# Performance work log

Measured on AMD Instinct MI355X. Metric: run time of the kernel, lower is better.

## Reference

```python
import jax, jax.numpy as jnp
import numpy as np

B, D, H = 524288, 256, 4
DH = D // H
LN_EPS = 1e-5


def setup_inputs() -> dict:
    key = jax.random.key(0)
    ks = jax.random.split(key, 3)
    s = 0.02  # typical init scale
    return {
        "x": jax.random.normal(ks[0], (B, 2, D), dtype=jnp.float32),
        "in_proj_w": jax.random.normal(ks[1], (3 * D, D), dtype=jnp.float32) * s,
        "in_proj_b": jnp.zeros((3 * D,), dtype=jnp.float32),
        "out_proj_w": jax.random.normal(ks[2], (D, D), dtype=jnp.float32) * s,
        "out_proj_b": jnp.zeros((D,), dtype=jnp.float32),
        "ln_gamma": jnp.ones((D,), dtype=jnp.float32),
        "ln_beta": jnp.zeros((D,), dtype=jnp.float32),
    }


def _mha_1to1(q, k, v, Wq, bq, Wk, bk, Wv, bv, Wo, bo):
    # q, k, v: [B, D]  (seq_len == 1 collapsed). Faithful MHA math.
    Q = (q @ Wq.T + bq).reshape(-1, H, DH)  # [B,H,DH]
    K = (k @ Wk.T + bk).reshape(-1, H, DH)
    V = (v @ Wv.T + bv).reshape(-1, H, DH)
    scores = jnp.sum(Q * K, axis=-1, keepdims=True) / np.sqrt(DH)  # [B,H,1]
    w = jax.nn.softmax(scores, axis=-1)  # softmax over a single key -> 1
    out = (w * V).reshape(-1, D)  # [B,D]
    return out @ Wo.T + bo


def reference(x, in_proj_w, in_proj_b, out_proj_w, out_proj_b, ln_gamma, ln_beta):
    Wq, Wk, Wv = jnp.split(in_proj_w, 3, axis=0)
    bq, bk, bv = jnp.split(in_proj_b, 3, axis=0)
    x0, x1 = x[:, 0, :], x[:, 1, :]
    out12 = _mha_1to1(x0, x1, x1, Wq, bq, Wk, bk, Wv, bv, out_proj_w, out_proj_b)
    out21 = _mha_1to1(x1, x0, x0, Wq, bq, Wk, bk, Wv, bv, out_proj_w, out_proj_b)
    fused = jnp.stack([out12, out21], axis=1)  # [B,2,D]
    y = x + fused  # dropout = identity in eval
    mu = jnp.mean(y, axis=-1, keepdims=True)
    var = jnp.var(y, axis=-1, keepdims=True)
    return (y - mu) * jax.lax.rsqrt(var + LN_EPS) * ln_gamma + ln_beta
```

## Files before the change

kernel.cpp:

```cpp
#include <hip/hip_runtime.h>

#define DD 256
#define TOTROWS (524288 * 2)
#define NBLOCKS 256
#define RPI 32
#define ITERS (TOTROWS / (NBLOCKS * RPI))
#define XROW 528
#define XBUF(i) ((i) * (RPI * XROW))
#define YBUF(i) (4 * RPI * XROW + (i) * (RPI * XROW))
#define LDS_TOTAL (6 * RPI * XROW)

typedef __attribute__((ext_vector_type(8))) short short8;
typedef __attribute__((ext_vector_type(4))) float f32x4;
typedef __attribute__((ext_vector_type(4))) unsigned short u16x4;

__device__ inline unsigned short f2bf(float x) {
    unsigned u = __builtin_bit_cast(unsigned, x);
    u += 0x7fffu + ((u >> 16) & 1u);
    return (unsigned short)(u >> 16);
}
__device__ inline float bf2f(unsigned short h) {
    unsigned u = ((unsigned)h) << 16;
    return __builtin_bit_cast(float, u);
}

__device__ inline void block_sync_lds() {
    __builtin_amdgcn_sched_barrier(0);
    asm volatile("s_waitcnt lgkmcnt(0)" ::: "memory");
    __builtin_amdgcn_s_barrier();
    __builtin_amdgcn_sched_barrier(0);
}

__global__ void wprep_kernel(const float* __restrict__ in_w,
                             const float* __restrict__ in_b,
                             const float* __restrict__ out_w,
                             const float* __restrict__ out_b,
                             unsigned short* __restrict__ Wbf,
                             float* __restrict__ cvec) {
    __shared__ float worow[DD];
    __shared__ float part[DD];
    const int i = blockIdx.x;
    const int j = threadIdx.x;
    worow[j] = out_w[i * DD + j];
    __syncthreads();
    const float* wv = in_w + 512 * DD;
    float s = 0.f;
    for (int k = 0; k < DD; ++k) s = fmaf(worow[k], wv[k * DD + j], s);
    Wbf[i * DD + j] = f2bf(s);
    part[j] = worow[j] * in_b[512 + j];
    __syncthreads();
    if (j == 0) {
        float c = out_b[i];
        for (int k = 0; k < DD; ++k) c += part[k];
        cvec[i] = c;
    }
}

__global__ __launch_bounds__(512, 2) void fused_kernel(
    const float* __restrict__ x, const unsigned short* __restrict__ Wbf,
    const float* __restrict__ cvec, const float* __restrict__ gamma,
    const float* __restrict__ beta, float* __restrict__ out) {
    extern __shared__ __align__(16) char lds[];
    const int tid = threadIdx.x;
    const int w = tid >> 6, lane = tid & 63;
    const int m = lane & 15, g = lane >> 4;
    const int lc = lane & 15, lr = tid >> 4;

    short8 af[2][8];
#pragma unroll
    for (int n2 = 0; n2 < 2; ++n2)
#pragma unroll
        for (int s = 0; s < 8; ++s)
            af[n2][s] = *(const short8*)(Wbf + (w * 32 + n2 * 16 + m) * 256 + s * 32 + g * 8);

    f32x4 creg[2];
#pragma unroll
    for (int n2 = 0; n2 < 2; ++n2)
        creg[n2] = *(const f32x4*)(cvec + w * 32 + n2 * 16 + g * 4);
    f32x4 gg[4], bb[4];
#pragma unroll
    for (int k = 0; k < 4; ++k) {
        gg[k] = *(const f32x4*)(gamma + lc * 4 + k * 64);
        bb[k] = *(const f32x4*)(beta + lc * 4 + k * 64);
    }

    const size_t rowbase = (size_t)blockIdx.x * (ITERS * RPI);

    f32x4 svA[4], svB[4];
#pragma unroll
    for (int j = 0; j < 4; ++j)
        svA[j] = *(const f32x4*)(x + rowbase * DD + j * 2048 + tid * 4);
#pragma unroll
    for (int j = 0; j < 4; ++j) {
        const int row = j * 8 + w;
        u16x4 h = {f2bf(svA[j][0]), f2bf(svA[j][1]), f2bf(svA[j][2]), f2bf(svA[j][3])};
        *(u16x4*)(lds + XBUF(0) + row * XROW + lane * 8) = h;
    }
#pragma unroll
    for (int j = 0; j < 4; ++j)
        svA[j] = *(const f32x4*)(x + (rowbase + RPI) * DD + j * 2048 + tid * 4);
#pragma unroll
    for (int j = 0; j < 4; ++j) {
        const int row = j * 8 + w;
        u16x4 h = {f2bf(svA[j][0]), f2bf(svA[j][1]), f2bf(svA[j][2]), f2bf(svA[j][3])};
        *(u16x4*)(lds + XBUF(1) + row * XROW + lane * 8) = h;
    }
#pragma unroll
    for (int j = 0; j < 4; ++j)
        svA[j] = *(const f32x4*)(x + (rowbase + 2 * RPI) * DD + j * 2048 + tid * 4);
    block_sync_lds();

#define REGION(IT, SVC, SVN)                                                     \
    {                                                                            \
        const int it = (IT);                                                     \
        const int xbc = XBUF(it & 3);                                            \
        const int xbs = XBUF((it + 2) & 3);                                      \
        const int ybA = YBUF(it & 1);                                            \
        const int ybB = YBUF((it + 1) & 1);                                      \
        const size_t r0 = rowbase + (size_t)it * RPI;                            \
                                           \
        if (it > 0) {                                                            \
            const size_t rp = r0 - RPI + lr;                                     \
            u16x4 yh[4];                                                         \
            _Pragma("unroll")                                                    \
            for (int k = 0; k < 4; ++k)                                          \
                yh[k] = *(const u16x4*)(lds + ybB + lr * XROW + lc * 8 + k * 128);\
            float s1 = 0.f, s2 = 0.f;                                            \
            float f[4][4];                                                       \
            _Pragma("unroll")                                                    \
            for (int k = 0; k < 4; ++k)                                          \
                _Pragma("unroll")                                                \
                for (int e = 0; e < 4; ++e) {                                    \
                    float v = bf2f(yh[k][e]);                                    \
                    f[k][e] = v;                                                 \
                    s1 += v;                                                     \
                    s2 = fmaf(v, v, s2);                                         \
                }                                                                \
            s1 += __shfl_xor(s1, 1); s2 += __shfl_xor(s2, 1);                    \
            s1 += __shfl_xor(s1, 2); s2 += __shfl_xor(s2, 2);                    \
            s1 += __shfl_xor(s1, 4); s2 += __shfl_xor(s2, 4);                    \
            s1 += __shfl_xor(s1, 8); s2 += __shfl_xor(s2, 8);                    \
            const float mu = s1 * (1.f / 256.f);                                 \
            const float var = s2 * (1.f / 256.f) - mu * mu;                      \
            const float rs = rsqrtf(var + 1e-5f);                                \
            _Pragma("unroll")                                                    \
            for (int k = 0; k < 4; ++k) {                                        \
                f32x4 o;                                                         \
                _Pragma("unroll")                                                \
                for (int e = 0; e < 4; ++e)                                      \
                    o[e] = fmaf((f[k][e] - mu) * rs, gg[k][e], bb[k][e]);        \
                __builtin_nontemporal_store(o, (f32x4*)(out + rp * DD + lc * 4 + k * 64)); \
            }                                                                    \
        }                                                                        \
                        \
        f32x4 acc[2][2];                                                         \
        acc[0][0] = f32x4{0.f, 0.f, 0.f, 0.f};                                   \
        acc[0][1] = f32x4{0.f, 0.f, 0.f, 0.f};                                   \
        acc[1][0] = f32x4{0.f, 0.f, 0.f, 0.f};                                   \
        acc[1][1] = f32x4{0.f, 0.f, 0.f, 0.f};                                   \
        _Pragma("unroll")                                                        \
        for (int t = 0; t < 2; ++t) {                                            \
            const int rowp = t * 16 + (m ^ 1);                                   \
            const char* bbase = lds + xbc + rowp * XROW + g * 16;                \
            _Pragma("unroll")                                                    \
            for (int s = 0; s < 8; ++s) {                                        \
                short8 bf_ = *(const short8*)(bbase + s * 64);                   \
                acc[t][0] = __builtin_amdgcn_mfma_f32_16x16x32_bf16(af[0][s], bf_, acc[t][0], 0, 0, 0); \
                acc[t][1] = __builtin_amdgcn_mfma_f32_16x16x32_bf16(af[1][s], bf_, acc[t][1], 0, 0, 0); \
            }                                                                    \
        }                                                                        \
        _Pragma("unroll")                                                        \
        for (int t = 0; t < 2; ++t) {                                            \
            const int rowm = t * 16 + m;                                         \
            _Pragma("unroll")                                                    \
            for (int n2 = 0; n2 < 2; ++n2) {                                     \
                u16x4 rh = *(const u16x4*)(lds + xbc + rowm * XROW + w * 64 + n2 * 32 + g * 8); \
                f32x4 y = acc[t][n2];                                            \
                _Pragma("unroll")                                                \
                for (int i = 0; i < 4; ++i) y[i] += bf2f(rh[i]) + creg[n2][i];   \
                u16x4 hy = {f2bf(y[0]), f2bf(y[1]), f2bf(y[2]), f2bf(y[3])};     \
                *(u16x4*)(lds + ybA + rowm * XROW + w * 64 + n2 * 32 + g * 8) = hy; \
            }                                                                    \
        }                                                                        \
                                           \
        if (it + 2 < ITERS) {                                                    \
            _Pragma("unroll")                                                    \
            for (int j = 0; j < 4; ++j) {                                        \
                const int row = j * 8 + w;                                       \
                u16x4 h = {f2bf(SVC[j][0]), f2bf(SVC[j][1]), f2bf(SVC[j][2]), f2bf(SVC[j][3])}; \
                *(u16x4*)(lds + xbs + row * XROW + lane * 8) = h;                \
            }                                                                    \
        }                                                                        \
                   \
        if (it + 3 < ITERS) {                                                    \
            _Pragma("unroll")                                                    \
            for (int j = 0; j < 4; ++j)                                          \
                SVN[j] = *(const f32x4*)(x + (r0 + 3 * RPI) * DD + j * 2048 + tid * 4); \
        }                                                                        \
        block_sync_lds();                                                        \
    }

    for (int itb = 0; itb < ITERS; itb += 2) {
        REGION(itb, svA, svB);
        REGION(itb + 1, svB, svA);
    }
#undef REGION

    {
        const int ybB = YBUF((ITERS - 1) & 1);
        const size_t rp = rowbase + (size_t)(ITERS - 1) * RPI + lr;
        u16x4 yh[4];
#pragma unroll
        for (int k = 0; k < 4; ++k)
            yh[k] = *(const u16x4*)(lds + ybB + lr * XROW + lc * 8 + k * 128);
        float s1 = 0.f, s2 = 0.f;
        float f[4][4];
#pragma unroll
        for (int k = 0; k < 4; ++k)
#pragma unroll
            for (int e = 0; e < 4; ++e) {
                float v = bf2f(yh[k][e]);
                f[k][e] = v;
                s1 += v;
                s2 = fmaf(v, v, s2);
            }
        s1 += __shfl_xor(s1, 1); s2 += __shfl_xor(s2, 1);
        s1 += __shfl_xor(s1, 2); s2 += __shfl_xor(s2, 2);
        s1 += __shfl_xor(s1, 4); s2 += __shfl_xor(s2, 4);
        s1 += __shfl_xor(s1, 8); s2 += __shfl_xor(s2, 8);
        const float mu = s1 * (1.f / 256.f);
        const float var = s2 * (1.f / 256.f) - mu * mu;
        const float rs = rsqrtf(var + 1e-5f);
#pragma unroll
        for (int k = 0; k < 4; ++k) {
            f32x4 o;
#pragma unroll
            for (int e = 0; e < 4; ++e)
                o[e] = fmaf((f[k][e] - mu) * rs, gg[k][e], bb[k][e]);
            __builtin_nontemporal_store(o, (f32x4*)(out + rp * DD + lc * 4 + k * 64));
        }
    }
}

extern "C" void kernel_launch(void* const* d_in, const int* in_sizes, int n_in,
                              void* d_out, int out_size, void* d_ws, size_t ws_size,
                              hipStream_t stream) {
    const float* x     = (const float*)d_in[0];
    const float* in_w  = (const float*)d_in[1];
    const float* in_b  = (const float*)d_in[2];
    const float* out_w = (const float*)d_in[3];
    const float* out_b = (const float*)d_in[4];
    const float* gamma = (const float*)d_in[5];
    const float* beta  = (const float*)d_in[6];
    float* out = (float*)d_out;

    unsigned short* Wbf = (unsigned short*)d_ws;
    float* cvec = (float*)((char*)d_ws + 131072);

    hipLaunchKernelGGL(wprep_kernel, dim3(256), dim3(256), 0, stream,
                       in_w, in_b, out_w, out_b, Wbf, cvec);

    hipFuncSetAttribute(reinterpret_cast<const void*>(fused_kernel),
                        hipFuncAttributeMaxDynamicSharedMemorySize, LDS_TOTAL);
    hipLaunchKernelGGL(fused_kernel, dim3(NBLOCKS), dim3(512), LDS_TOTAL, stream,
                       x, Wbf, cvec, gamma, beta, out);
}
```

Baseline: 419.2 us.

## Stagger per-wave-pair phase order to overlap LN, MFMA, staging and loads

Each iteration's four phases (LayerNorm output, MFMA projection, bf16 staging into LDS, global prefetch) are split into macros. Each pair of waves (grp = tid>>7) runs them in a different rotated order, so at any moment different waves hit different units (VMEM, MFMA, LDS, VALU). The aim is to avoid every wave contending for the same resource at once between barriers. The switch makes the code larger and can raise register pressure, and the loop only stays correct because all four orders remain inside the same barrier region.

```diff
diff --git a/kernel.cpp b/kernel.cpp
--- a/kernel.cpp
+++ b/kernel.cpp
@@ -63,6 +63,7 @@
     extern __shared__ __align__(16) char lds[];
     const int tid = threadIdx.x;
     const int w = tid >> 6, lane = tid & 63;
+    const int grp = tid >> 7;
     const int m = lane & 15, g = lane >> 4;
     const int lc = lane & 15, lr = tid >> 4;
 
@@ -109,6 +110,91 @@
     for (int j = 0; j < 4; ++j)
         svA[j] = *(const f32x4*)(x + (rowbase + 2 * RPI) * DD + j * 2048 + tid * 4);
     block_sync_lds();
+
+#define P_LN                                                                     \
+    if (it > 0) {                                                                \
+        const size_t rp = r0 - RPI + lr;                                         \
+        u16x4 yh[4];                                                             \
+        _Pragma("unroll")                                                        \
+        for (int k = 0; k < 4; ++k)                                              \
+            yh[k] = *(const u16x4*)(lds + ybB + lr * XROW + lc * 8 + k * 128);   \
+        float s1 = 0.f, s2 = 0.f;                                                \
+        float fv[4][4];                                                          \
+        _Pragma("unroll")                                                        \
+        for (int k = 0; k < 4; ++k)                                              \
+            _Pragma("unroll")                                                    \
+            for (int e = 0; e < 4; ++e) {                                        \
+                float v = bf2f(yh[k][e]);                                        \
+                fv[k][e] = v;                                                    \
+                s1 += v;                                                         \
+                s2 = fmaf(v, v, s2);                                             \
+            }                                                                    \
+        s1 += __shfl_xor(s1, 1); s2 += __shfl_xor(s2, 1);                        \
+        s1 += __shfl_xor(s1, 2); s2 += __shfl_xor(s2, 2);                        \
+        s1 += __shfl_xor(s1, 4); s2 += __shfl_xor(s2, 4);                        \
+        s1 += __shfl_xor(s1, 8); s2 += __shfl_xor(s2, 8);                        \
+        const float mu = s1 * (1.f / 256.f);                                     \
+        const float var = s2 * (1.f / 256.f) - mu * mu;                          \
+        const float rs = rsqrtf(var + 1e-5f);                                    \
+        _Pragma("unroll")                                                        \
+        for (int k = 0; k < 4; ++k) {                                            \
+            f32x4 o;                                                             \
+            _Pragma("unroll")                                                    \
+            for (int e = 0; e < 4; ++e)                                          \
+                o[e] = fmaf((fv[k][e] - mu) * rs, gg[k][e], bb[k][e]);           \
+            __builtin_nontemporal_store(o, (f32x4*)(out + rp * DD + lc * 4 + k * 64)); \
+        }                                                                        \
+    }
+
+#define P_MFMA                                                                   \
+    {                                                                            \
+        f32x4 acc[2][2];                                                         \
+        acc[0][0] = f32x4{0.f, 0.f, 0.f, 0.f};                                   \
+        acc[0][1] = f32x4{0.f, 0.f, 0.f, 0.f};                                   \
+        acc[1][0] = f32x4{0.f, 0.f, 0.f, 0.f};                                   \
+        acc[1][1] = f32x4{0.f, 0.f, 0.f, 0.f};                                   \
+        _Pragma("unroll")                                                        \
+        for (int t = 0; t < 2; ++t) {                                            \
+            const int rowp = t * 16 + (m ^ 1);                                   \
+            const char* bbase = lds + xbc + rowp * XROW + g * 16;                \
+            _Pragma("unroll")                                                    \
+            for (int s = 0; s < 8; ++s) {                                        \
+                short8 bf_ = *(const short8*)(bbase + s * 64);                   \
+                acc[t][0] = __builtin_amdgcn_mfma_f32_16x16x32_bf16(af[0][s], bf_, acc[t][0], 0, 0, 0); \
+                acc[t][1] = __builtin_amdgcn_mfma_f32_16x16x32_bf16(af[1][s], bf_, acc[t][1], 0, 0, 0); \
+            }                                                                    \
+        }                                                                        \
+        _Pragma("unroll")                                                        \
+        for (int t = 0; t < 2; ++t) {                                            \
+            const int rowm = t * 16 + m;                                         \
+            _Pragma("unroll")                                                    \
+            for (int n2 = 0; n2 < 2; ++n2) {                                     \
+                u16x4 rh = *(const u16x4*)(lds + xbc + rowm * XROW + w * 64 + n2 * 32 + g * 8); \
+                f32x4 y = acc[t][n2];                                            \
+                _Pragma("unroll")                                                \
+                for (int i = 0; i < 4; ++i) y[i] += bf2f(rh[i]) + creg[n2][i];   \
+                u16x4 hy = {f2bf(y[0]), f2bf(y[1]), f2bf(y[2]), f2bf(y[3])};     \
+                *(u16x4*)(lds + ybA + rowm * XROW + w * 64 + n2 * 32 + g * 8) = hy; \
+            }                                                                    \
+        }                                                                        \
+    }
+
+#define P_STAGE(SVC)                                                             \
+    if (it + 2 < ITERS) {                                                        \
+        _Pragma("unroll")                                                        \
+        for (int j = 0; j < 4; ++j) {                                            \
+            const int row = j * 8 + w;                                           \
+            u16x4 h = {f2bf(SVC[j][0]), f2bf(SVC[j][1]), f2bf(SVC[j][2]), f2bf(SVC[j][3])}; \
+            *(u16x4*)(lds + xbs + row * XROW + lane * 8) = h;                    \
+        }                                                                        \
+    }
+
+#define P_LOAD(SVN)                                                              \
+    if (it + 3 < ITERS) {                                                        \
+        _Pragma("unroll")                                                        \
+        for (int j = 0; j < 4; ++j)                                              \
+            SVN[j] = *(const f32x4*)(x + (r0 + 3 * RPI) * DD + j * 2048 + tid * 4); \
+    }
 
 #define REGION(IT, SVC, SVN)                                                     \
     {                                                                            \
@@ -118,84 +204,11 @@
         const int ybA = YBUF(it & 1);                                            \
         const int ybB = YBUF((it + 1) & 1);                                      \
         const size_t r0 = rowbase + (size_t)it * RPI;                            \
-                                           \
-        if (it > 0) {                                                            \
-            const size_t rp = r0 - RPI + lr;                                     \
-            u16x4 yh[4];                                                         \
-            _Pragma("unroll")                                                    \
-            for (int k = 0; k < 4; ++k)                                          \
-                yh[k] = *(const u16x4*)(lds + ybB + lr * XROW + lc * 8 + k * 128);\
-            float s1 = 0.f, s2 = 0.f;                                            \
-            float f[4][4];                                                       \
-            _Pragma("unroll")                                                    \
-            for (int k = 0; k < 4; ++k)                                          \
-                _Pragma("unroll")                                                \
-                for (int e = 0; e < 4; ++e) {                                    \
-                    float v = bf2f(yh[k][e]);                                    \
-                    f[k][e] = v;                                                 \
-                    s1 += v;                                                     \
-                    s2 = fmaf(v, v, s2);                                         \
-                }                                                                \
-            s1 += __shfl_xor(s1, 1); s2 += __shfl_xor(s2, 1);                    \
-            s1 += __shfl_xor(s1, 2); s2 += __shfl_xor(s2, 2);                    \
-            s1 += __shfl_xor(s1, 4); s2 += __shfl_xor(s2, 4);                    \
-            s1 += __shfl_xor(s1, 8); s2 += __shfl_xor(s2, 8);                    \
-            const float mu = s1 * (1.f / 256.f);                                 \
-            const float var = s2 * (1.f / 256.f) - mu * mu;                      \
-            const float rs = rsqrtf(var + 1e-5f);                                \
-            _Pragma("unroll")                                                    \
-            for (int k = 0; k < 4; ++k) {                                        \
-                f32x4 o;                                                         \
-                _Pragma("unroll")                                                \
-                for (int e = 0; e < 4; ++e)                                      \
-                    o[e] = fmaf((f[k][e] - mu) * rs, gg[k][e], bb[k][e]);        \
-                __builtin_nontemporal_store(o, (f32x4*)(out + rp * DD + lc * 4 + k * 64)); \
-            }                                                                    \
-        }                                                                        \
-                        \
-        f32x4 acc[2][2];                                                         \
-        acc[0][0] = f32x4{0.f, 0.f, 0.f, 0.f};                                   \
-        acc[0][1] = f32x4{0.f, 0.f, 0.f, 0.f};                                   \
-        acc[1][0] = f32x4{0.f, 0.f, 0.f, 0.f};                                   \
-        acc[1][1] = f32x4{0.f, 0.f, 0.f, 0.f};                                   \
-        _Pragma("unroll")                                                        \
-        for (int t = 0; t < 2; ++t) {                                            \
-            const int rowp = t * 16 + (m ^ 1);                                   \
-            const char* bbase = lds + xbc + rowp * XROW + g * 16;                \
-            _Pragma("unroll")                                                    \
-            for (int s = 0; s < 8; ++s) {                                        \
-                short8 bf_ = *(const short8*)(bbase + s * 64);                   \
-                acc[t][0] = __builtin_amdgcn_mfma_f32_16x16x32_bf16(af[0][s], bf_, acc[t][0], 0, 0, 0); \
-                acc[t][1] = __builtin_amdgcn_mfma_f32_16x16x32_bf16(af[1][s], bf_, acc[t][1], 0, 0, 0); \
-            }                                                                    \
-        }                                                                        \
-        _Pragma("unroll")                                                        \
-        for (int t = 0; t < 2; ++t) {                                            \
-            const int rowm = t * 16 + m;                                         \
-            _Pragma("unroll")                                                    \
-            for (int n2 = 0; n2 < 2; ++n2) {                                     \
-                u16x4 rh = *(const u16x4*)(lds + xbc + rowm * XROW + w * 64 + n2 * 32 + g * 8); \
-                f32x4 y = acc[t][n2];                                            \
-                _Pragma("unroll")                                                \
-                for (int i = 0; i < 4; ++i) y[i] += bf2f(rh[i]) + creg[n2][i];   \
-                u16x4 hy = {f2bf(y[0]), f2bf(y[1]), f2bf(y[2]), f2bf(y[3])};     \
-                *(u16x4*)(lds + ybA + rowm * XROW + w * 64 + n2 * 32 + g * 8) = hy; \
-            }                                                                    \
-        }                                                                        \
-                                           \
-        if (it + 2 < ITERS) {                                                    \
-            _Pragma("unroll")                                                    \
-            for (int j = 0; j < 4; ++j) {                                        \
-                const int row = j * 8 + w;                                       \
-                u16x4 h = {f2bf(SVC[j][0]), f2bf(SVC[j][1]), f2bf(SVC[j][2]), f2bf(SVC[j][3])}; \
-                *(u16x4*)(lds + xbs + row * XROW + lane * 8) = h;                \
-            }                                                                    \
-        }                                                                        \
-                   \
-        if (it + 3 < ITERS) {                                                    \
-            _Pragma("unroll")                                                    \
-            for (int j = 0; j < 4; ++j)                                          \
-                SVN[j] = *(const f32x4*)(x + (r0 + 3 * RPI) * DD + j * 2048 + tid * 4); \
+        switch (grp) {                                                           \
+            case 0: { P_LN } P_MFMA P_STAGE(SVC) P_LOAD(SVN) break;              \
+            case 1: P_MFMA P_STAGE(SVC) P_LOAD(SVN) { P_LN } break;              \
+            case 2: P_STAGE(SVC) P_LOAD(SVN) { P_LN } P_MFMA break;              \
+            default: P_LOAD(SVN) { P_LN } P_MFMA P_STAGE(SVC) break;             \
         }                                                                        \
         block_sync_lds();                                                        \
     }
@@ -205,6 +218,10 @@
         REGION(itb + 1, svB, svA);
     }
 #undef REGION
+#undef P_LN
+#undef P_MFMA
+#undef P_STAGE
+#undef P_LOAD
 
     {
         const int ybB = YBUF((ITERS - 1) & 1);
@@ -214,13 +231,13 @@
         for (int k = 0; k < 4; ++k)
             yh[k] = *(const u16x4*)(lds + ybB + lr * XROW + lc * 8 + k * 128);
         float s1 = 0.f, s2 = 0.f;
-        float f[4][4];
+        float fv[4][4];
 #pragma unroll
         for (int k = 0; k < 4; ++k)
 #pragma unroll
             for (int e = 0; e < 4; ++e) {
                 float v = bf2f(yh[k][e]);
-                f[k][e] = v;
+                fv[k][e] = v;
                 s1 += v;
                 s2 = fmaf(v, v, s2);
             }
@@ -236,7 +253,7 @@
             f32x4 o;
 #pragma unroll
             for (int e = 0; e < 4; ++e)
-                o[e] = fmaf((f[k][e] - mu) * rs, gg[k][e], bb[k][e]);
+                o[e] = fmaf((fv[k][e] - mu) * rs, gg[k][e], bb[k][e]);
             __builtin_nontemporal_store(o, (f32x4*)(out + rp * DD + lc * 4 + k * 64));
         }
     }
```

Result: slower. 448.9 us (+7.1%).

## Keep GEMM outputs in registers and compute LayerNorm via LDS partial sums

Applied to the files above, without the earlier changes.

The y tile is no longer round-tripped through LDS as bf16. Accumulators stay in registers across iterations, and per-row partial sums and sum-of-squares go to a small LDS area that is reduced into mean and rstd for the epilogue. Rows per iteration double to 64, block count doubles, and x buffering drops from 4 to 2 stages with a one-iteration prefetch. bf16 packing now uses v_cvt_pk_bf16_f32. The cost is an extra block barrier per iteration, higher register pressure from two 4x2 accumulator sets, and shallower prefetch. As a side effect, y is no longer rounded to bf16 before normalization.

```diff
diff --git a/kernel.cpp b/kernel.cpp
--- a/kernel.cpp
+++ b/kernel.cpp
@@ -2,17 +2,20 @@
 
 #define DD 256
 #define TOTROWS (524288 * 2)
-#define NBLOCKS 256
-#define RPI 32
+#define NBLOCKS 512
+#define RPI 64
 #define ITERS (TOTROWS / (NBLOCKS * RPI))
 #define XROW 528
 #define XBUF(i) ((i) * (RPI * XROW))
-#define YBUF(i) (4 * RPI * XROW + (i) * (RPI * XROW))
-#define LDS_TOTAL (6 * RPI * XROW)
+#define SUMSB (2 * RPI * XROW)
+#define MURSB (SUMSB + RPI * 72)
+#define LDS_TOTAL (MURSB + RPI * 8)
 
 typedef __attribute__((ext_vector_type(8))) short short8;
 typedef __attribute__((ext_vector_type(4))) float f32x4;
+typedef __attribute__((ext_vector_type(2))) float f32x2;
 typedef __attribute__((ext_vector_type(4))) unsigned short u16x4;
+typedef __attribute__((ext_vector_type(2))) unsigned int u32x2;
 
 __device__ inline unsigned short f2bf(float x) {
     unsigned u = __builtin_bit_cast(unsigned, x);
@@ -22,6 +25,11 @@
 __device__ inline float bf2f(unsigned short h) {
     unsigned u = ((unsigned)h) << 16;
     return __builtin_bit_cast(float, u);
+}
+__device__ inline unsigned cvtpk(float lo, float hi) {
+    unsigned r;
+    asm("v_cvt_pk_bf16_f32 %0, %1, %2" : "=v"(r) : "v"(lo), "v"(hi));
+    return r;
 }
 
 __device__ inline void block_sync_lds() {
@@ -64,7 +72,7 @@
     const int tid = threadIdx.x;
     const int w = tid >> 6, lane = tid & 63;
     const int m = lane & 15, g = lane >> 4;
-    const int lc = lane & 15, lr = tid >> 4;
+    const int ar = tid >> 3, ap = tid & 7;
 
     short8 af[2][8];
 #pragma unroll
@@ -73,171 +81,158 @@
         for (int s = 0; s < 8; ++s)
             af[n2][s] = *(const short8*)(Wbf + (w * 32 + n2 * 16 + m) * 256 + s * 32 + g * 8);
 
-    f32x4 creg[2];
-#pragma unroll
-    for (int n2 = 0; n2 < 2; ++n2)
-        creg[n2] = *(const f32x4*)(cvec + w * 32 + n2 * 16 + g * 4);
-    f32x4 gg[4], bb[4];
-#pragma unroll
-    for (int k = 0; k < 4; ++k) {
-        gg[k] = *(const f32x4*)(gamma + lc * 4 + k * 64);
-        bb[k] = *(const f32x4*)(beta + lc * 4 + k * 64);
+    f32x4 creg[2], gg[2], bbv[2];
+#pragma unroll
+    for (int n2 = 0; n2 < 2; ++n2) {
+        const int c0 = w * 32 + n2 * 16 + g * 4;
+        creg[n2] = *(const f32x4*)(cvec + c0);
+        gg[n2]   = *(const f32x4*)(gamma + c0);
+        bbv[n2]  = *(const f32x4*)(beta + c0);
     }
 
     const size_t rowbase = (size_t)blockIdx.x * (ITERS * RPI);
 
-    f32x4 svA[4], svB[4];
-#pragma unroll
-    for (int j = 0; j < 4; ++j)
-        svA[j] = *(const f32x4*)(x + rowbase * DD + j * 2048 + tid * 4);
-#pragma unroll
-    for (int j = 0; j < 4; ++j) {
+    f32x4 sv[8];
+    f32x4 accA[4][2], accB[4][2];
+
+#pragma unroll
+    for (int j = 0; j < 8; ++j)
+        sv[j] = *(const f32x4*)(x + rowbase * DD + j * 2048 + tid * 4);
+#pragma unroll
+    for (int j = 0; j < 8; ++j) {
         const int row = j * 8 + w;
-        u16x4 h = {f2bf(svA[j][0]), f2bf(svA[j][1]), f2bf(svA[j][2]), f2bf(svA[j][3])};
-        *(u16x4*)(lds + XBUF(0) + row * XROW + lane * 8) = h;
-    }
-#pragma unroll
-    for (int j = 0; j < 4; ++j)
-        svA[j] = *(const f32x4*)(x + (rowbase + RPI) * DD + j * 2048 + tid * 4);
-#pragma unroll
-    for (int j = 0; j < 4; ++j) {
-        const int row = j * 8 + w;
-        u16x4 h = {f2bf(svA[j][0]), f2bf(svA[j][1]), f2bf(svA[j][2]), f2bf(svA[j][3])};
-        *(u16x4*)(lds + XBUF(1) + row * XROW + lane * 8) = h;
-    }
-#pragma unroll
-    for (int j = 0; j < 4; ++j)
-        svA[j] = *(const f32x4*)(x + (rowbase + 2 * RPI) * DD + j * 2048 + tid * 4);
+        u32x2 h = {cvtpk(sv[j][0], sv[j][1]), cvtpk(sv[j][2], sv[j][3])};
+        *(u32x2*)(lds + XBUF(0) + row * XROW + lane * 8) = h;
+    }
+#pragma unroll
+    for (int j = 0; j < 8; ++j)
+        sv[j] = *(const f32x4*)(x + (rowbase + RPI) * DD + j * 2048 + tid * 4);
     block_sync_lds();
 
-#define REGION(IT, SVC, SVN)                                                     \
+#define REGION(IT, ACCP, ACCC)                                                   \
     {                                                                            \
         const int it = (IT);                                                     \
-        const int xbc = XBUF(it & 3);                                            \
-        const int xbs = XBUF((it + 2) & 3);                                      \
-        const int ybA = YBUF(it & 1);                                            \
-        const int ybB = YBUF((it + 1) & 1);                                      \
+        const int xbc = XBUF(it & 1);                                            \
+        const int xbn = XBUF((it + 1) & 1);                                      \
         const size_t r0 = rowbase + (size_t)it * RPI;                            \
-                                           \
+            \
         if (it > 0) {                                                            \
-            const size_t rp = r0 - RPI + lr;                                     \
-            u16x4 yh[4];                                                         \
-            _Pragma("unroll")                                                    \
-            for (int k = 0; k < 4; ++k)                                          \
-                yh[k] = *(const u16x4*)(lds + ybB + lr * XROW + lc * 8 + k * 128);\
-            float s1 = 0.f, s2 = 0.f;                                            \
-            float f[4][4];                                                       \
-            _Pragma("unroll")                                                    \
-            for (int k = 0; k < 4; ++k)                                          \
+            f32x2 p = *(const f32x2*)(lds + SUMSB + ar * 72 + ap * 8);           \
+            float a = p[0], b = p[1];                                            \
+            a += __shfl_xor(a, 1); b += __shfl_xor(b, 1);                        \
+            a += __shfl_xor(a, 2); b += __shfl_xor(b, 2);                        \
+            a += __shfl_xor(a, 4); b += __shfl_xor(b, 4);                        \
+            if (ap == 0) {                                                       \
+                const float mu = a * (1.f / 256.f);                              \
+                const float var = b * (1.f / 256.f) - mu * mu;                   \
+                *(f32x2*)(lds + MURSB + ar * 8) = f32x2{mu, rsqrtf(var + 1e-5f)};\
+            }                                                                    \
+        }                                                                        \
+        block_sync_lds();                                             \
+                     \
+        if (it > 0) {                                                            \
+            const size_t r0p = r0 - RPI;                                         \
+            _Pragma("unroll")                                                    \
+            for (int t = 0; t < 4; ++t) {                                        \
+                f32x2 mr = *(const f32x2*)(lds + MURSB + (t * 16 + m) * 8);      \
                 _Pragma("unroll")                                                \
-                for (int e = 0; e < 4; ++e) {                                    \
-                    float v = bf2f(yh[k][e]);                                    \
-                    f[k][e] = v;                                                 \
-                    s1 += v;                                                     \
-                    s2 = fmaf(v, v, s2);                                         \
+                for (int n2 = 0; n2 < 2; ++n2) {                                 \
+                    f32x4 y = ACCP[t][n2], o;                                    \
+                    _Pragma("unroll")                                            \
+                    for (int i = 0; i < 4; ++i)                                  \
+                        o[i] = fmaf((y[i] - mr[0]) * mr[1], gg[n2][i], bbv[n2][i]); \
+                    __builtin_nontemporal_store(o,                               \
+                        (f32x4*)(out + (r0p + t * 16 + m) * DD + w * 32 + n2 * 16 + g * 4)); \
                 }                                                                \
-            s1 += __shfl_xor(s1, 1); s2 += __shfl_xor(s2, 1);                    \
-            s1 += __shfl_xor(s1, 2); s2 += __shfl_xor(s2, 2);                    \
-            s1 += __shfl_xor(s1, 4); s2 += __shfl_xor(s2, 4);                    \
-            s1 += __shfl_xor(s1, 8); s2 += __shfl_xor(s2, 8);                    \
-            const float mu = s1 * (1.f / 256.f);                                 \
-            const float var = s2 * (1.f / 256.f) - mu * mu;                      \
-            const float rs = rsqrtf(var + 1e-5f);                                \
-            _Pragma("unroll")                                                    \
-            for (int k = 0; k < 4; ++k) {                                        \
-                f32x4 o;                                                         \
-                _Pragma("unroll")                                                \
-                for (int e = 0; e < 4; ++e)                                      \
-                    o[e] = fmaf((f[k][e] - mu) * rs, gg[k][e], bb[k][e]);        \
-                __builtin_nontemporal_store(o, (f32x4*)(out + rp * DD + lc * 4 + k * 64)); \
-            }                                                                    \
-        }                                                                        \
-                        \
-        f32x4 acc[2][2];                                                         \
-        acc[0][0] = f32x4{0.f, 0.f, 0.f, 0.f};                                   \
-        acc[0][1] = f32x4{0.f, 0.f, 0.f, 0.f};                                   \
-        acc[1][0] = f32x4{0.f, 0.f, 0.f, 0.f};                                   \
-        acc[1][1] = f32x4{0.f, 0.f, 0.f, 0.f};                                   \
+            }                                                                    \
+        }                                                                        \
+         \
         _Pragma("unroll")                                                        \
-        for (int t = 0; t < 2; ++t) {                                            \
+        for (int t = 0; t < 4; ++t) {                                            \
+            ACCC[t][0] = creg[0];                                                \
+            ACCC[t][1] = creg[1];                                                \
+        }                                                                        \
+        _Pragma("unroll")                                                        \
+        for (int t = 0; t < 4; ++t) {                                            \
             const int rowp = t * 16 + (m ^ 1);                                   \
             const char* bbase = lds + xbc + rowp * XROW + g * 16;                \
             _Pragma("unroll")                                                    \
             for (int s = 0; s < 8; ++s) {                                        \
                 short8 bf_ = *(const short8*)(bbase + s * 64);                   \
-                acc[t][0] = __builtin_amdgcn_mfma_f32_16x16x32_bf16(af[0][s], bf_, acc[t][0], 0, 0, 0); \
-                acc[t][1] = __builtin_amdgcn_mfma_f32_16x16x32_bf16(af[1][s], bf_, acc[t][1], 0, 0, 0); \
+                ACCC[t][0] = __builtin_amdgcn_mfma_f32_16x16x32_bf16(af[0][s], bf_, ACCC[t][0], 0, 0, 0); \
+                ACCC[t][1] = __builtin_amdgcn_mfma_f32_16x16x32_bf16(af[1][s], bf_, ACCC[t][1], 0, 0, 0); \
             }                                                                    \
         }                                                                        \
         _Pragma("unroll")                                                        \
-        for (int t = 0; t < 2; ++t) {                                            \
+        for (int t = 0; t < 4; ++t) {                                            \
             const int rowm = t * 16 + m;                                         \
+            float s1 = 0.f, s2 = 0.f;                                            \
             _Pragma("unroll")                                                    \
             for (int n2 = 0; n2 < 2; ++n2) {                                     \
                 u16x4 rh = *(const u16x4*)(lds + xbc + rowm * XROW + w * 64 + n2 * 32 + g * 8); \
-                f32x4 y = acc[t][n2];                                            \
+                f32x4 y = ACCC[t][n2];                                           \
                 _Pragma("unroll")                                                \
-                for (int i = 0; i < 4; ++i) y[i] += bf2f(rh[i]) + creg[n2][i];   \
-                u16x4 hy = {f2bf(y[0]), f2bf(y[1]), f2bf(y[2]), f2bf(y[3])};     \
-                *(u16x4*)(lds + ybA + rowm * XROW + w * 64 + n2 * 32 + g * 8) = hy; \
-            }                                                                    \
-        }                                                                        \
-                                           \
+                for (int i = 0; i < 4; ++i) y[i] += bf2f(rh[i]);                 \
+                ACCC[t][n2] = y;                                                 \
+                _Pragma("unroll")                                                \
+                for (int i = 0; i < 4; ++i) {                                    \
+                    s1 += y[i];                                                  \
+                    s2 = fmaf(y[i], y[i], s2);                                   \
+                }                                                                \
+            }                                                                    \
+            s1 += __shfl_xor(s1, 16); s2 += __shfl_xor(s2, 16);                  \
+            s1 += __shfl_xor(s1, 32); s2 += __shfl_xor(s2, 32);                  \
+            if (g == 0)                                                          \
+                *(f32x2*)(lds + SUMSB + rowm * 72 + w * 8) = f32x2{s1, s2};      \
+        }                                                                        \
+                  \
+        if (it + 1 < ITERS) {                                                    \
+            _Pragma("unroll")                                                    \
+            for (int j = 0; j < 8; ++j) {                                        \
+                const int row = j * 8 + w;                                       \
+                u32x2 h = {cvtpk(sv[j][0], sv[j][1]), cvtpk(sv[j][2], sv[j][3])};\
+                *(u32x2*)(lds + xbn + row * XROW + lane * 8) = h;                \
+            }                                                                    \
+        }                                                                        \
         if (it + 2 < ITERS) {                                                    \
             _Pragma("unroll")                                                    \
-            for (int j = 0; j < 4; ++j) {                                        \
-                const int row = j * 8 + w;                                       \
-                u16x4 h = {f2bf(SVC[j][0]), f2bf(SVC[j][1]), f2bf(SVC[j][2]), f2bf(SVC[j][3])}; \
-                *(u16x4*)(lds + xbs + row * XROW + lane * 8) = h;                \
-            }                                                                    \
-        }                                                                        \
-                   \
-        if (it + 3 < ITERS) {                                                    \
-            _Pragma("unroll")                                                    \
-            for (int j = 0; j < 4; ++j)                                          \
-                SVN[j] = *(const f32x4*)(x + (r0 + 3 * RPI) * DD + j * 2048 + tid * 4); \
-        }                                                                        \
-        block_sync_lds();                                                        \
+            for (int j = 0; j < 8; ++j)                                          \
+                sv[j] = *(const f32x4*)(x + (r0 + 2 * RPI) * DD + j * 2048 + tid * 4); \
+        }                                                                        \
+        block_sync_lds();                                              \
     }
 
     for (int itb = 0; itb < ITERS; itb += 2) {
-        REGION(itb, svA, svB);
-        REGION(itb + 1, svB, svA);
+        REGION(itb, accB, accA);
+        REGION(itb + 1, accA, accB);
     }
 #undef REGION
 
     {
-        const int ybB = YBUF((ITERS - 1) & 1);
-        const size_t rp = rowbase + (size_t)(ITERS - 1) * RPI + lr;
-        u16x4 yh[4];
-#pragma unroll
-        for (int k = 0; k < 4; ++k)
-            yh[k] = *(const u16x4*)(lds + ybB + lr * XROW + lc * 8 + k * 128);
-        float s1 = 0.f, s2 = 0.f;
-        float f[4][4];
-#pragma unroll
-        for (int k = 0; k < 4; ++k)
-#pragma unroll
-            for (int e = 0; e < 4; ++e) {
-                float v = bf2f(yh[k][e]);
-                f[k][e] = v;
-                s1 += v;
-                s2 = fmaf(v, v, s2);
+        f32x2 p = *(const f32x2*)(lds + SUMSB + ar * 72 + ap * 8);
+        float a = p[0], b = p[1];
+        a += __shfl_xor(a, 1); b += __shfl_xor(b, 1);
+        a += __shfl_xor(a, 2); b += __shfl_xor(b, 2);
+        a += __shfl_xor(a, 4); b += __shfl_xor(b, 4);
+        if (ap == 0) {
+            const float mu = a * (1.f / 256.f);
+            const float var = b * (1.f / 256.f) - mu * mu;
+            *(f32x2*)(lds + MURSB + ar * 8) = f32x2{mu, rsqrtf(var + 1e-5f)};
+        }
+        block_sync_lds();
+        const size_t r0p = rowbase + (size_t)(ITERS - 1) * RPI;
+#pragma unroll
+        for (int t = 0; t < 4; ++t) {
+            f32x2 mr = *(const f32x2*)(lds + MURSB + (t * 16 + m) * 8);
+#pragma unroll
+            for (int n2 = 0; n2 < 2; ++n2) {
+                f32x4 y = accB[t][n2], o;
+#pragma unroll
+                for (int i = 0; i < 4; ++i)
+                    o[i] = fmaf((y[i] - mr[0]) * mr[1], gg[n2][i], bbv[n2][i]);
+                __builtin_nontemporal_store(o,
+                    (f32x4*)(out + (r0p + t * 16 + m) * DD + w * 32 + n2 * 16 + g * 4));
             }
-        s1 += __shfl_xor(s1, 1); s2 += __shfl_xor(s2, 1);
-        s1 += __shfl_xor(s1, 2); s2 += __shfl_xor(s2, 2);
-        s1 += __shfl_xor(s1, 4); s2 += __shfl_xor(s2, 4);
-        s1 += __shfl_xor(s1, 8); s2 += __shfl_xor(s2, 8);
-        const float mu = s1 * (1.f / 256.f);
-        const float var = s2 * (1.f / 256.f) - mu * mu;
-        const float rs = rsqrtf(var + 1e-5f);
-#pragma unroll
-        for (int k = 0; k < 4; ++k) {
-            f32x4 o;
-#pragma unroll
-            for (int e = 0; e < 4; ++e)
-                o[e] = fmaf((f[k][e] - mu) * rs, gg[k][e], bb[k][e]);
-            __builtin_nontemporal_store(o, (f32x4*)(out + rp * DD + lc * 4 + k * 64));
         }
     }
 }
```

Measured after the change: 557.5 us. 33.0% more time.
